# Kernel tuning notes

Hardware: AMD Instinct MI355X
Metric: run time of the kernel (lower is better)

## Reference

```python
import jax, jax.numpy as jnp
import numpy as np
import math

B, S, D = 2, 2048, 1024
H, HKV, HD = 16, 4, 64
SF = 4
SD = HD // SF  # sparsity proj dim = 16
TEMP = 1.0
INIT_STD = 0.02


def rope(qk):
    # qk: [b, h, s, d]
    d = qk.shape[-1]
    theta = 1.0 / (10000.0 ** (jnp.arange(0, d, 2, dtype=jnp.float32) / d))  # [d/2]
    s = jnp.arange(qk.shape[2], dtype=jnp.float32)
    freqs = jnp.outer(s, theta)                     # [s, d/2]
    freqs = jnp.concatenate([freqs, freqs], -1)     # [s, d]
    qk1, qk2 = jnp.split(qk, 2, axis=-1)
    rot = jnp.concatenate([-qk2, qk1], -1)
    return qk * jnp.cos(freqs) + rot * jnp.sin(freqs)


def setup_inputs() -> dict:
    key = jax.random.key(0)
    ks = jax.random.split(key, 8)
    x = jax.random.normal(ks[0], (B, S, D), dtype=jnp.float32)
    Wq = jax.random.normal(ks[1], (D, D), dtype=jnp.float32) * INIT_STD
    Wk = jax.random.normal(ks[2], (HKV * HD, D), dtype=jnp.float32) * INIT_STD
    Wv = jax.random.normal(ks[3], (HKV * HD, D), dtype=jnp.float32) * INIT_STD
    Wo = jax.random.normal(ks[4], (D, D), dtype=jnp.float32) * INIT_STD
    bo = jnp.zeros((D,), dtype=jnp.float32)
    Ws = jax.random.normal(ks[5], (SD, HD), dtype=jnp.float32) * INIT_STD
    bs = jnp.zeros((SD,), dtype=jnp.float32)
    return {"x": x, "Wq": Wq, "Wk": Wk, "Wv": Wv, "Wo": Wo, "bo": bo, "Ws": Ws, "bs": bs}


def reference(x, Wq, Wk, Wv, Wo, bo, Ws, bs):
    b, s, _ = x.shape
    # projections (torch Linear: x @ W.T)
    q = (x @ Wq.T).reshape(b, s, H, HD).transpose(0, 2, 1, 3)     # [b,H,s,hd]
    k = (x @ Wk.T).reshape(b, s, HKV, HD).transpose(0, 2, 1, 3)   # [b,Hkv,s,hd]
    v = (x @ Wv.T).reshape(b, s, HKV, HD).transpose(0, 2, 1, 3)
    q = rope(q)
    k = rope(k)
    n_rep = H // HKV
    k = jnp.repeat(k, n_rep, axis=1)  # [b,H,s,hd]
    v = jnp.repeat(v, n_rep, axis=1)
    # low-rank sparsity gate
    q_sp = q @ Ws.T + bs              # [b,H,s,sd]
    k_sp = k @ Ws.T + bs
    sp_scores = jnp.einsum('bhid,bhjd->bhij', q_sp, k_sp) / math.sqrt(SD)
    gate = jax.nn.sigmoid(sp_scores / TEMP)
    attn = jnp.einsum('bhid,bhjd->bhij', q, k) / math.sqrt(HD)
    attn = attn * gate
    causal = jnp.triu(jnp.ones((s, s), dtype=bool), k=1)
    attn = jnp.where(causal, -jnp.inf, attn)
    w = jax.nn.softmax(attn, axis=-1)
    out = jnp.einsum('bhij,bhjd->bhid', w, v)               # [b,H,s,hd]
    out = out.transpose(0, 2, 1, 3).reshape(b, s, H * HD)   # [b,s,D]
    return out @ Wo.T + bo
```

## Files before the change

kernel.cpp:

```cpp
#include <hip/hip_runtime.h>
#include <math.h>

#define B_ 2
#define S_ 2048
#define D_ 1024
#define H_ 16
#define HKV_ 4
#define HD_ 64
#define SD_ 16

typedef __attribute__((ext_vector_type(8))) short bf16x8;
typedef __attribute__((ext_vector_type(4))) float f32x4;
typedef __attribute__((ext_vector_type(8))) unsigned short us8;
typedef __attribute__((ext_vector_type(4))) unsigned short us4;

#define LOG2E 1.4426950408889634f

__device__ __forceinline__ unsigned short f2bf(float f) {
  unsigned int u = __builtin_bit_cast(unsigned int, f);
  u += 0x7fffu + ((u >> 16) & 1u);
  return (unsigned short)(u >> 16);
}

__device__ __forceinline__ void gload16(const unsigned short* g, unsigned short* l) {
  __builtin_amdgcn_global_load_lds(
      (const __attribute__((address_space(1))) unsigned int*)g,
      (__attribute__((address_space(3))) unsigned int*)l, 16, 0, 0);
}

__global__ __launch_bounds__(256) void convert_bf16(
    const float* __restrict__ x, const float* __restrict__ wq,
    const float* __restrict__ wk, const float* __restrict__ wv,
    const float* __restrict__ wo, unsigned short* __restrict__ xb,
    unsigned short* __restrict__ wqkv, unsigned short* __restrict__ wob) {
  const int blk = blockIdx.x;
  const float* src;
  unsigned short* dst;
  int off;
  if (blk < 2048)      { src = x;  dst = xb;             off = blk * 2048; }
  else if (blk < 2560) { src = wq; dst = wqkv;           off = (blk - 2048) * 2048; }
  else if (blk < 2688) { src = wk; dst = wqkv + 1048576; off = (blk - 2560) * 2048; }
  else if (blk < 2816) { src = wv; dst = wqkv + 1310720; off = (blk - 2688) * 2048; }
  else                 { src = wo; dst = wob;            off = (blk - 2816) * 2048; }
  const int i = off + threadIdx.x * 8;
  float4 a = *(const float4*)(src + i);
  float4 b = *(const float4*)(src + i + 4);
  us8 o;
  o[0] = f2bf(a.x); o[1] = f2bf(a.y); o[2] = f2bf(a.z); o[3] = f2bf(a.w);
  o[4] = f2bf(b.x); o[5] = f2bf(b.y); o[6] = f2bf(b.z); o[7] = f2bf(b.w);
  *(us8*)(dst + i) = o;
}

__global__ __launch_bounds__(256) void gemm_bf16(
    const unsigned short* __restrict__ A, const unsigned short* __restrict__ Bm,
    const float* __restrict__ bias, float* __restrict__ C, int N) {
  __shared__ unsigned short As[64 * 64];
  __shared__ unsigned short Bs[128 * 64];
  const int tid = threadIdx.x;
  const int w = tid >> 6, lane = tid & 63;
  const int nm = lane & 15, quad = lane >> 4;
  const int m0 = blockIdx.y * 64, n0 = blockIdx.x * 128;
  const int wn = w * 32;

  f32x4 acc[4][2] = {};
  int arow[2], acol[2], brow[4], bcol[4];
#pragma unroll
  for (int it = 0; it < 2; ++it) {
    int s = it * 256 + tid;
    arow[it] = s >> 3;
    acol[it] = ((s & 7) ^ (arow[it] & 7)) * 8;
  }
#pragma unroll
  for (int it = 0; it < 4; ++it) {
    int s = it * 256 + tid;
    brow[it] = s >> 3;
    bcol[it] = ((s & 7) ^ (brow[it] & 7)) * 8;
  }

  for (int k0 = 0; k0 < 1024; k0 += 64) {
    __syncthreads();
#pragma unroll
    for (int it = 0; it < 2; ++it)
      gload16(A + (size_t)(m0 + arow[it]) * 1024 + k0 + acol[it],
              &As[(it * 256 + w * 64) * 8]);
#pragma unroll
    for (int it = 0; it < 4; ++it)
      gload16(Bm + (size_t)(n0 + brow[it]) * 1024 + k0 + bcol[it],
              &Bs[(it * 256 + w * 64) * 8]);
    __syncthreads();

#pragma unroll
    for (int ks = 0; ks < 2; ++ks) {
      const int cq = ks * 4 + quad;
      bf16x8 af[4], bfr[2];
#pragma unroll
      for (int mi = 0; mi < 4; ++mi) {
        const int m = mi * 16 + nm;
        af[mi] = *(const bf16x8*)&As[(m * 8 + (cq ^ (m & 7))) * 8];
      }
#pragma unroll
      for (int ni = 0; ni < 2; ++ni) {
        const int n = wn + ni * 16 + nm;
        bfr[ni] = *(const bf16x8*)&Bs[(n * 8 + (cq ^ (n & 7))) * 8];
      }
#pragma unroll
      for (int mi = 0; mi < 4; ++mi)
#pragma unroll
        for (int ni = 0; ni < 2; ++ni)
          acc[mi][ni] = __builtin_amdgcn_mfma_f32_16x16x32_bf16(
              af[mi], bfr[ni], acc[mi][ni], 0, 0, 0);
    }
  }

  float bv[2] = {0.f, 0.f};
  if (bias) {
#pragma unroll
    for (int ni = 0; ni < 2; ++ni) bv[ni] = bias[n0 + wn + ni * 16 + nm];
  }
#pragma unroll
  for (int mi = 0; mi < 4; ++mi) {
#pragma unroll
    for (int r = 0; r < 4; ++r) {
      const int row = m0 + mi * 16 + quad * 4 + r;
      float* crow = C + (size_t)row * N + n0 + wn + nm;
#pragma unroll
      for (int ni = 0; ni < 2; ++ni) crow[ni * 16] = acc[mi][ni][r] + bv[ni];
    }
  }
}

__global__ __launch_bounds__(256) void rope_scatter(
    const float* __restrict__ P, const float* __restrict__ Ws,
    const float* __restrict__ bs, unsigned short* __restrict__ qh,
    unsigned short* __restrict__ kh, unsigned short* __restrict__ qsp,
    unsigned short* __restrict__ ksp) {
  __shared__ float wsl[16 * 64];
  __shared__ float bsl[16];
  __shared__ float rbuf[4][64];
  const int tid = threadIdx.x;
  const int row = blockIdx.x;
  const int b = row >> 11;
  const int s = row & 2047;
  {
    *(float4*)&wsl[tid * 4] = *(const float4*)&Ws[tid * 4];
    if (tid < 16) bsl[tid] = bs[tid];
  }
  __syncthreads();
  const int w = tid >> 6, lane = tid & 63;
  const int i = lane & 31, halfu = lane >> 5;
  const float theta = powf(10000.f, -((float)(2 * i) * (1.f / 64.f)));
  const float f = (float)s * theta;
  const float cf = cosf(f);
  const float sf = sinf(f);
  for (int slot = w; slot < 20; slot += 4) {
    float val = P[(size_t)row * 1536 + slot * 64 + lane];
    float partner = __shfl_xor(val, 32);
    float rot = halfu ? partner : -partner;
    float r = val * cf + rot * sf;
    unsigned short* dst;
    unsigned short* spdst;
    float qscale, spscale;
    if (slot < 16) {
      dst = qh + ((size_t)(b * 16 + slot) * 2048 + s) * 64;
      spdst = qsp + ((size_t)(b * 16 + slot) * 2048 + s) * 16;
      qscale = 0.125f * LOG2E; spscale = 0.25f * LOG2E;
    } else {
      int hh = slot - 16;
      dst = kh + ((size_t)(b * 4 + hh) * 2048 + s) * 64;
      spdst = ksp + ((size_t)(b * 4 + hh) * 2048 + s) * 16;
      qscale = 1.f; spscale = 1.f;
    }
    dst[lane] = f2bf(r * qscale);
    rbuf[w][lane] = r;
    int p = lane >> 4, j = lane & 15;
    float partial = 0.f;
#pragma unroll
    for (int t = 0; t < 16; ++t)
      partial += wsl[j * 64 + p * 16 + t] * rbuf[w][p * 16 + t];
    partial += __shfl_xor(partial, 16);
    partial += __shfl_xor(partial, 32);
    if (p == 0) spdst[j] = f2bf((partial + bsl[j]) * spscale);
  }
}

__global__ __launch_bounds__(256) void v_transpose(
    const float* __restrict__ proj, unsigned short* __restrict__ vt) {
  __shared__ unsigned short t_[64 * 72];
  const int bkv = blockIdx.y;
  const int s0 = blockIdx.x * 64;
  const int b = bkv >> 2, hkv = bkv & 3;
  const int tid = threadIdx.x;
  const int sl = tid >> 2;
  const int c0 = (tid & 3) * 16;
  const float* src = proj + ((size_t)b * 2048 + s0 + sl) * 1536 + 1280 + hkv * 64 + c0;
  us8 o0, o1;
#pragma unroll
  for (int t = 0; t < 8; ++t) { o0[t] = f2bf(src[t]); o1[t] = f2bf(src[8 + t]); }
  *(us8*)&t_[sl * 72 + c0] = o0;
  *(us8*)&t_[sl * 72 + c0 + 8] = o1;
  __syncthreads();
  const int d = tid >> 2;
  const int sc_ = (tid & 3) * 16;
  us8 w0, w1;
#pragma unroll
  for (int t = 0; t < 8; ++t) w0[t] = t_[(sc_ + t) * 72 + d];
#pragma unroll
  for (int t = 0; t < 8; ++t) w1[t] = t_[(sc_ + 8 + t) * 72 + d];
  unsigned short* dst = vt + (size_t)bkv * 131072 + (size_t)d * 2048 + s0 + sc_;
  *(us8*)dst = w0;
  *(us8*)(dst + 8) = w1;
}

__global__ __launch_bounds__(256) void attn_kernel(
    const unsigned short* __restrict__ qh, const unsigned short* __restrict__ kh,
    const unsigned short* __restrict__ vt, const unsigned short* __restrict__ qsp,
    const unsigned short* __restrict__ ksp, unsigned short* __restrict__ ao) {
  __shared__ unsigned short Ks[64 * 64];
  __shared__ unsigned short Vs[64 * 64];
  __shared__ unsigned short Ksp[64 * 16];
  __shared__ unsigned short Pw[4][16 * 64];

  const int tid = threadIdx.x;
  const int w = tid >> 6;
  const int lane = tid & 63;
  const int nm = lane & 15;
  const int quad = lane >> 4;
  const int bh = blockIdx.y;
  const int b = bh >> 4, h = bh & 15;
  const int hkv = h >> 2;
  const size_t kbase = (size_t)(b * 4 + hkv) * 2048 * 64;
  const size_t vbase = (size_t)(b * 4 + hkv) * 131072;
  const size_t kspb = (size_t)(b * 4 + hkv) * 2048 * 16;

  int srow_[2], scol_[2];
#pragma unroll
  for (int rd = 0; rd < 2; ++rd) {
    int Lc = rd * 256 + w * 64 + lane;
    int r = Lc >> 3;
    srow_[rd] = r;
    scol_[rd] = ((Lc & 7) ^ (r & 7)) * 8;
  }
  unsigned short* pw = &Pw[w][0];

  for (int ph = 0; ph < 2; ++ph) {
    const int qx = ph ? blockIdx.x : (31 - blockIdx.x);
    const int q0 = qx * 64;
    const int qrow0 = q0 + w * 16;

    const size_t qb = ((size_t)(b * 16 + h) * 2048 + qrow0 + nm) * 64;
    bf16x8 qa0 = *(const bf16x8*)(qh + qb + quad * 8);
    bf16x8 qa1 = *(const bf16x8*)(qh + qb + 32 + quad * 8);
    bf16x8 qspa = {0, 0, 0, 0, 0, 0, 0, 0};
    if (quad < 2)
      qspa = *(const bf16x8*)(qsp + ((size_t)(b * 16 + h) * 2048 + qrow0 + nm) * 16 + quad * 8);

    float l_r[4] = {0.f, 0.f, 0.f, 0.f};
    f32x4 O[4] = {{0.f, 0.f, 0.f, 0.f}, {0.f, 0.f, 0.f, 0.f},
                  {0.f, 0.f, 0.f, 0.f}, {0.f, 0.f, 0.f, 0.f}};

    const int ntile = qx + 1;
    for (int jt = 0; jt < ntile; ++jt) {
      const int j0 = jt * 64;
      __syncthreads();
#pragma unroll
      for (int rd = 0; rd < 2; ++rd) {
        gload16(kh + kbase + (size_t)(j0 + srow_[rd]) * 64 + scol_[rd],
                &Ks[(rd * 256 + w * 64) * 8]);
        gload16(vt + vbase + (size_t)srow_[rd] * 2048 + j0 + scol_[rd],
                &Vs[(rd * 256 + w * 64) * 8]);
      }
      if (w < 2) {
        const int Lc = w * 64 + lane;
        gload16(ksp + kspb + (size_t)(j0 + (Lc >> 1)) * 16 + (Lc & 1) * 8,
                &Ksp[w * 512]);
      }
      __syncthreads();

      const bool needmask = (j0 + 63 > qrow0);
#pragma unroll
      for (int st = 0; st < 4; ++st) {
        if (j0 + st * 16 > qrow0 + 15) {
#pragma unroll
          for (int r = 0; r < 4; ++r) {
            const int prow = quad * 4 + r;
            const int chunk = (st * 2 + (nm >> 3)) ^ (prow & 7);
            pw[(prow * 8 + chunk) * 8 + (nm & 7)] = 0;
          }
          continue;
        }
        const int krow = st * 16 + nm;
        const int r7 = krow & 7;
        bf16x8 kb0 = *(const bf16x8*)&Ks[(krow * 8 + (quad ^ r7)) * 8];
        bf16x8 kb1 = *(const bf16x8*)&Ks[(krow * 8 + ((4 + quad) ^ r7)) * 8];
        bf16x8 gb = *(const bf16x8*)&Ksp[(krow * 2 + (quad & 1)) * 8];
        f32x4 z = {0.f, 0.f, 0.f, 0.f};
        f32x4 s = __builtin_amdgcn_mfma_f32_16x16x32_bf16(qa0, kb0, z, 0, 0, 0);
        s = __builtin_amdgcn_mfma_f32_16x16x32_bf16(qa1, kb1, s, 0, 0, 0);
        f32x4 g = __builtin_amdgcn_mfma_f32_16x16x32_bf16(qspa, gb, z, 0, 0, 0);
        const bool edge = (j0 + st * 16 + 15 > qrow0);
#pragma unroll
        for (int r = 0; r < 4; ++r) {
          float gate = __builtin_amdgcn_rcpf(1.f + __builtin_amdgcn_exp2f(-g[r]));
          float v = s[r] * gate;
          if (edge) {
            const int col = j0 + st * 16 + nm;
            const int rowg = qrow0 + quad * 4 + r;
            v = (col > rowg) ? -INFINITY : v;
          }
          float p = __builtin_amdgcn_exp2f(v);
          l_r[r] += p;
          const int prow = quad * 4 + r;
          const int chunk = (st * 2 + (nm >> 3)) ^ (prow & 7);
          pw[(prow * 8 + chunk) * 8 + (nm & 7)] = f2bf(p);
        }
      }

#pragma unroll
      for (int c = 0; c < 2; ++c) {
        const int gc = c * 4 + quad;
        bf16x8 pa = *(const bf16x8*)&pw[(nm * 8 + (gc ^ (nm & 7))) * 8];
#pragma unroll
        for (int dt = 0; dt < 4; ++dt) {
          const int vrow = dt * 16 + nm;
          bf16x8 vb = *(const bf16x8*)&Vs[(vrow * 8 + (gc ^ (vrow & 7))) * 8];
          O[dt] = __builtin_amdgcn_mfma_f32_16x16x32_bf16(pa, vb, O[dt], 0, 0, 0);
        }
      }
    }

#pragma unroll
    for (int r = 0; r < 4; ++r) {
      float v = l_r[r];
      v += __shfl_xor(v, 1);
      v += __shfl_xor(v, 2);
      v += __shfl_xor(v, 4);
      v += __shfl_xor(v, 8);
      const float inv = __builtin_amdgcn_rcpf(v);
      const int rowg = qrow0 + quad * 4 + r;
      unsigned short* orow = ao + ((size_t)b * 2048 + rowg) * 1024 + h * 64 + nm;
#pragma unroll
      for (int dt = 0; dt < 4; ++dt) orow[dt * 16] = f2bf(O[dt][r] * inv);
    }
  }
}

extern "C" void kernel_launch(void* const* d_in, const int* in_sizes, int n_in,
                              void* d_out, int out_size, void* d_ws,
                              size_t ws_size, hipStream_t stream) {
  const float* x = (const float*)d_in[0];
  const float* Wq = (const float*)d_in[1];
  const float* Wk = (const float*)d_in[2];
  const float* Wv = (const float*)d_in[3];
  const float* Wo = (const float*)d_in[4];
  const float* bo = (const float*)d_in[5];
  const float* Ws = (const float*)d_in[6];
  const float* bs = (const float*)d_in[7];
  float* out = (float*)d_out;

  char* wsb = (char*)d_ws;
  float* proj = (float*)wsb;
  unsigned short* aob  = (unsigned short*)wsb;
  unsigned short* qh   = (unsigned short*)(wsb + 25165824);
  unsigned short* kh   = (unsigned short*)(wsb + 33554432);
  unsigned short* vtb  = (unsigned short*)(wsb + 35651584);
  unsigned short* qsp  = (unsigned short*)(wsb + 37748736);
  unsigned short* ksp  = (unsigned short*)(wsb + 39845888);
  unsigned short* xb   = (unsigned short*)(wsb + 40370176);
  unsigned short* wqkv = (unsigned short*)(wsb + 48758784);
  unsigned short* wob  = (unsigned short*)(wsb + 51904512);

  convert_bf16<<<dim3(3328), 256, 0, stream>>>(x, Wq, Wk, Wv, Wo, xb, wqkv, wob);
  gemm_bf16<<<dim3(12, 64), 256, 0, stream>>>(xb, wqkv, nullptr, proj, 1536);
  rope_scatter<<<dim3(4096), 256, 0, stream>>>(proj, Ws, bs, qh, kh, qsp, ksp);
  v_transpose<<<dim3(32, 8), 256, 0, stream>>>(proj, vtb);
  attn_kernel<<<dim3(16, 32), 256, 0, stream>>>(qh, kh, vtb, qsp, ksp, aob);
  gemm_bf16<<<dim3(8, 64), 256, 0, stream>>>(aob, wob, bo, out, 1024);
}
```

Before: 203.5 us.

## Double-buffer K/V/Ksp tiles in attention kernel with one barrier per tile

Splits the shared K, V and Ksp tiles into two buffers and prefetches the next tile while the current one is computed, dropping one of the two barriers per iteration. Both query phases now run as one continuous pipeline, with the first tile of the second phase prefetched during the last tile of the first phase. This is meant to hide global-to-LDS load latency behind MFMA work. In exchange it doubles LDS use for K/V, which may lower occupancy, and relies on gload16 being asynchronous for the overlap to happen.

```diff
diff --git a/kernel.cpp b/kernel.cpp
--- a/kernel.cpp
+++ b/kernel.cpp
@@ -211,13 +211,69 @@
   *(us8*)(dst + 8) = w1;
 }
 
+__device__ __forceinline__ void attn_tile(
+    const unsigned short* __restrict__ Ksb, const unsigned short* __restrict__ Vsb,
+    const unsigned short* __restrict__ Kspb_, unsigned short* __restrict__ pw,
+    bf16x8 qa0, bf16x8 qa1, bf16x8 qspa, int j0, int qrow0, int nm, int quad,
+    float l_r[4], f32x4 O[4]) {
+#pragma unroll
+  for (int st = 0; st < 4; ++st) {
+    if (j0 + st * 16 > qrow0 + 15) {
+#pragma unroll
+      for (int r = 0; r < 4; ++r) {
+        const int prow = quad * 4 + r;
+        const int chunk = (st * 2 + (nm >> 3)) ^ (prow & 7);
+        pw[(prow * 8 + chunk) * 8 + (nm & 7)] = 0;
+      }
+      continue;
+    }
+    const int krow = st * 16 + nm;
+    const int r7 = krow & 7;
+    bf16x8 kb0 = *(const bf16x8*)&Ksb[(krow * 8 + (quad ^ r7)) * 8];
+    bf16x8 kb1 = *(const bf16x8*)&Ksb[(krow * 8 + ((4 + quad) ^ r7)) * 8];
+    bf16x8 gb = *(const bf16x8*)&Kspb_[(krow * 2 + (quad & 1)) * 8];
+    f32x4 z = {0.f, 0.f, 0.f, 0.f};
+    f32x4 s = __builtin_amdgcn_mfma_f32_16x16x32_bf16(qa0, kb0, z, 0, 0, 0);
+    s = __builtin_amdgcn_mfma_f32_16x16x32_bf16(qa1, kb1, s, 0, 0, 0);
+    f32x4 g = __builtin_amdgcn_mfma_f32_16x16x32_bf16(qspa, gb, z, 0, 0, 0);
+    const bool edge = (j0 + st * 16 + 15 > qrow0);
+#pragma unroll
+    for (int r = 0; r < 4; ++r) {
+      float gate = __builtin_amdgcn_rcpf(1.f + __builtin_amdgcn_exp2f(-g[r]));
+      float v = s[r] * gate;
+      if (edge) {
+        const int col = j0 + st * 16 + nm;
+        const int rowg = qrow0 + quad * 4 + r;
+        v = (col > rowg) ? -INFINITY : v;
+      }
+      float p = __builtin_amdgcn_exp2f(v);
+      l_r[r] += p;
+      const int prow = quad * 4 + r;
+      const int chunk = (st * 2 + (nm >> 3)) ^ (prow & 7);
+      pw[(prow * 8 + chunk) * 8 + (nm & 7)] = f2bf(p);
+    }
+  }
+
+#pragma unroll
+  for (int c = 0; c < 2; ++c) {
+    const int gc = c * 4 + quad;
+    bf16x8 pa = *(const bf16x8*)&pw[(nm * 8 + (gc ^ (nm & 7))) * 8];
+#pragma unroll
+    for (int dt = 0; dt < 4; ++dt) {
+      const int vrow = dt * 16 + nm;
+      bf16x8 vb = *(const bf16x8*)&Vsb[(vrow * 8 + (gc ^ (vrow & 7))) * 8];
+      O[dt] = __builtin_amdgcn_mfma_f32_16x16x32_bf16(pa, vb, O[dt], 0, 0, 0);
+    }
+  }
+}
+
 __global__ __launch_bounds__(256) void attn_kernel(
     const unsigned short* __restrict__ qh, const unsigned short* __restrict__ kh,
     const unsigned short* __restrict__ vt, const unsigned short* __restrict__ qsp,
     const unsigned short* __restrict__ ksp, unsigned short* __restrict__ ao) {
-  __shared__ unsigned short Ks[64 * 64];
-  __shared__ unsigned short Vs[64 * 64];
-  __shared__ unsigned short Ksp[64 * 16];
+  __shared__ unsigned short Ks[2][64 * 64];
+  __shared__ unsigned short Vs[2][64 * 64];
+  __shared__ unsigned short Ksp[2][64 * 16];
   __shared__ unsigned short Pw[4][16 * 64];
 
   const int tid = threadIdx.x;
@@ -242,106 +298,95 @@
   }
   unsigned short* pw = &Pw[w][0];
 
-  for (int ph = 0; ph < 2; ++ph) {
-    const int qx = ph ? blockIdx.x : (31 - blockIdx.x);
-    const int q0 = qx * 64;
-    const int qrow0 = q0 + w * 16;
-
-    const size_t qb = ((size_t)(b * 16 + h) * 2048 + qrow0 + nm) * 64;
-    bf16x8 qa0 = *(const bf16x8*)(qh + qb + quad * 8);
-    bf16x8 qa1 = *(const bf16x8*)(qh + qb + 32 + quad * 8);
-    bf16x8 qspa = {0, 0, 0, 0, 0, 0, 0, 0};
-    if (quad < 2)
-      qspa = *(const bf16x8*)(qsp + ((size_t)(b * 16 + h) * 2048 + qrow0 + nm) * 16 + quad * 8);
-
-    float l_r[4] = {0.f, 0.f, 0.f, 0.f};
-    f32x4 O[4] = {{0.f, 0.f, 0.f, 0.f}, {0.f, 0.f, 0.f, 0.f},
-                  {0.f, 0.f, 0.f, 0.f}, {0.f, 0.f, 0.f, 0.f}};
-
-    const int ntile = qx + 1;
-    for (int jt = 0; jt < ntile; ++jt) {
-      const int j0 = jt * 64;
-      __syncthreads();
-#pragma unroll
-      for (int rd = 0; rd < 2; ++rd) {
-        gload16(kh + kbase + (size_t)(j0 + srow_[rd]) * 64 + scol_[rd],
-                &Ks[(rd * 256 + w * 64) * 8]);
-        gload16(vt + vbase + (size_t)srow_[rd] * 2048 + j0 + scol_[rd],
-                &Vs[(rd * 256 + w * 64) * 8]);
-      }
-      if (w < 2) {
-        const int Lc = w * 64 + lane;
-        gload16(ksp + kspb + (size_t)(j0 + (Lc >> 1)) * 16 + (Lc & 1) * 8,
-                &Ksp[w * 512]);
-      }
-      __syncthreads();
-
-      const bool needmask = (j0 + 63 > qrow0);
-#pragma unroll
-      for (int st = 0; st < 4; ++st) {
-        if (j0 + st * 16 > qrow0 + 15) {
-#pragma unroll
-          for (int r = 0; r < 4; ++r) {
-            const int prow = quad * 4 + r;
-            const int chunk = (st * 2 + (nm >> 3)) ^ (prow & 7);
-            pw[(prow * 8 + chunk) * 8 + (nm & 7)] = 0;
-          }
-          continue;
-        }
-        const int krow = st * 16 + nm;
-        const int r7 = krow & 7;
-        bf16x8 kb0 = *(const bf16x8*)&Ks[(krow * 8 + (quad ^ r7)) * 8];
-        bf16x8 kb1 = *(const bf16x8*)&Ks[(krow * 8 + ((4 + quad) ^ r7)) * 8];
-        bf16x8 gb = *(const bf16x8*)&Ksp[(krow * 2 + (quad & 1)) * 8];
-        f32x4 z = {0.f, 0.f, 0.f, 0.f};
-        f32x4 s = __builtin_amdgcn_mfma_f32_16x16x32_bf16(qa0, kb0, z, 0, 0, 0);
-        s = __builtin_amdgcn_mfma_f32_16x16x32_bf16(qa1, kb1, s, 0, 0, 0);
-        f32x4 g = __builtin_amdgcn_mfma_f32_16x16x32_bf16(qspa, gb, z, 0, 0, 0);
-        const bool edge = (j0 + st * 16 + 15 > qrow0);
-#pragma unroll
-        for (int r = 0; r < 4; ++r) {
-          float gate = __builtin_amdgcn_rcpf(1.f + __builtin_amdgcn_exp2f(-g[r]));
-          float v = s[r] * gate;
-          if (edge) {
-            const int col = j0 + st * 16 + nm;
-            const int rowg = qrow0 + quad * 4 + r;
-            v = (col > rowg) ? -INFINITY : v;
-          }
-          float p = __builtin_amdgcn_exp2f(v);
-          l_r[r] += p;
-          const int prow = quad * 4 + r;
-          const int chunk = (st * 2 + (nm >> 3)) ^ (prow & 7);
-          pw[(prow * 8 + chunk) * 8 + (nm & 7)] = f2bf(p);
-        }
-      }
-
-#pragma unroll
-      for (int c = 0; c < 2; ++c) {
-        const int gc = c * 4 + quad;
-        bf16x8 pa = *(const bf16x8*)&pw[(nm * 8 + (gc ^ (nm & 7))) * 8];
-#pragma unroll
-        for (int dt = 0; dt < 4; ++dt) {
-          const int vrow = dt * 16 + nm;
-          bf16x8 vb = *(const bf16x8*)&Vs[(vrow * 8 + (gc ^ (vrow & 7))) * 8];
-          O[dt] = __builtin_amdgcn_mfma_f32_16x16x32_bf16(pa, vb, O[dt], 0, 0, 0);
-        }
-      }
-    }
-
-#pragma unroll
-    for (int r = 0; r < 4; ++r) {
-      float v = l_r[r];
-      v += __shfl_xor(v, 1);
-      v += __shfl_xor(v, 2);
-      v += __shfl_xor(v, 4);
-      v += __shfl_xor(v, 8);
-      const float inv = __builtin_amdgcn_rcpf(v);
-      const int rowg = qrow0 + quad * 4 + r;
-      unsigned short* orow = ao + ((size_t)b * 2048 + rowg) * 1024 + h * 64 + nm;
-#pragma unroll
-      for (int dt = 0; dt < 4; ++dt) orow[dt * 16] = f2bf(O[dt][r] * inv);
-    }
-  }
+#define STAGE(BUF, J0)                                                         \
+  {                                                                            \
+    _Pragma("unroll")                                                          \
+    for (int rd = 0; rd < 2; ++rd) {                                           \
+      gload16(kh + kbase + (size_t)((J0) + srow_[rd]) * 64 + scol_[rd],        \
+              &Ks[BUF][(rd * 256 + w * 64) * 8]);                              \
+      gload16(vt + vbase + (size_t)srow_[rd] * 2048 + (J0) + scol_[rd],        \
+              &Vs[BUF][(rd * 256 + w * 64) * 8]);                              \
+    }                                                                          \
+    if (w < 2) {                                                               \
+      const int Lc = w * 64 + lane;                                            \
+      gload16(ksp + kspb + (size_t)((J0) + (Lc >> 1)) * 16 + (Lc & 1) * 8,     \
+              &Ksp[BUF][w * 512]);                                             \
+    }                                                                          \
+  }
+
+  const int qxA = 31 - blockIdx.x;
+  const int qxB = blockIdx.x;
+  const int qrow0A = qxA * 64 + w * 16;
+  const int qrow0B = qxB * 64 + w * 16;
+
+  const size_t qbA = ((size_t)(b * 16 + h) * 2048 + qrow0A + nm) * 64;
+  bf16x8 qa0A = *(const bf16x8*)(qh + qbA + quad * 8);
+  bf16x8 qa1A = *(const bf16x8*)(qh + qbA + 32 + quad * 8);
+  const size_t qbB = ((size_t)(b * 16 + h) * 2048 + qrow0B + nm) * 64;
+  bf16x8 qa0B = *(const bf16x8*)(qh + qbB + quad * 8);
+  bf16x8 qa1B = *(const bf16x8*)(qh + qbB + 32 + quad * 8);
+  bf16x8 qspaA = {0, 0, 0, 0, 0, 0, 0, 0};
+  bf16x8 qspaB = {0, 0, 0, 0, 0, 0, 0, 0};
+  if (quad < 2) {
+    qspaA = *(const bf16x8*)(qsp + ((size_t)(b * 16 + h) * 2048 + qrow0A + nm) * 16 + quad * 8);
+    qspaB = *(const bf16x8*)(qsp + ((size_t)(b * 16 + h) * 2048 + qrow0B + nm) * 16 + quad * 8);
+  }
+
+  float l_r[4] = {0.f, 0.f, 0.f, 0.f};
+  f32x4 O[4] = {{0.f, 0.f, 0.f, 0.f}, {0.f, 0.f, 0.f, 0.f},
+                {0.f, 0.f, 0.f, 0.f}, {0.f, 0.f, 0.f, 0.f}};
+
+  STAGE(0, 0);
+  int cur = 0;
+  for (int jt = 0; jt <= qxA; ++jt) {
+    __syncthreads();
+    if (jt < qxA) STAGE(cur ^ 1, (jt + 1) * 64)
+    else          STAGE(cur ^ 1, 0)
+    attn_tile(&Ks[cur][0], &Vs[cur][0], &Ksp[cur][0], pw,
+              qa0A, qa1A, qspaA, jt * 64, qrow0A, nm, quad, l_r, O);
+    cur ^= 1;
+  }
+
+#pragma unroll
+  for (int r = 0; r < 4; ++r) {
+    float v = l_r[r];
+    v += __shfl_xor(v, 1);
+    v += __shfl_xor(v, 2);
+    v += __shfl_xor(v, 4);
+    v += __shfl_xor(v, 8);
+    const float inv = __builtin_amdgcn_rcpf(v);
+    const int rowg = qrow0A + quad * 4 + r;
+    unsigned short* orow = ao + ((size_t)b * 2048 + rowg) * 1024 + h * 64 + nm;
+#pragma unroll
+    for (int dt = 0; dt < 4; ++dt) orow[dt * 16] = f2bf(O[dt][r] * inv);
+  }
+#pragma unroll
+  for (int dt = 0; dt < 4; ++dt) O[dt] = (f32x4){0.f, 0.f, 0.f, 0.f};
+#pragma unroll
+  for (int r = 0; r < 4; ++r) l_r[r] = 0.f;
+
+  for (int jt = 0; jt <= qxB; ++jt) {
+    __syncthreads();
+    if (jt < qxB) STAGE(cur ^ 1, (jt + 1) * 64)
+    attn_tile(&Ks[cur][0], &Vs[cur][0], &Ksp[cur][0], pw,
+              qa0B, qa1B, qspaB, jt * 64, qrow0B, nm, quad, l_r, O);
+    cur ^= 1;
+  }
+
+#pragma unroll
+  for (int r = 0; r < 4; ++r) {
+    float v = l_r[r];
+    v += __shfl_xor(v, 1);
+    v += __shfl_xor(v, 2);
+    v += __shfl_xor(v, 4);
+    v += __shfl_xor(v, 8);
+    const float inv = __builtin_amdgcn_rcpf(v);
+    const int rowg = qrow0B + quad * 4 + r;
+    unsigned short* orow = ao + ((size_t)b * 2048 + rowg) * 1024 + h * 64 + nm;
+#pragma unroll
+    for (int dt = 0; dt < 4; ++dt) orow[dt * 16] = f2bf(O[dt][r] * inv);
+  }
+#undef STAGE
 }
 
 extern "C" void kernel_launch(void* const* d_in, const int* in_sizes, int n_in,
```

After: 207.1 us. Within noise of the previous version (+1.8%).
